# Optimization experiments

Hardware: AMD Instinct MI355X
Metric: run time of the kernel (lower is better)

## Reference

```python
import jax, jax.numpy as jnp
import numpy as np

B, IN, OUT = 512, 4096, 11008


def setup_inputs() -> dict:
    key = jax.random.key(0)
    k_x, k_stored, k_sign, k_scale, k_bias = jax.random.split(key, 5)
    x = jax.random.normal(k_x, (B, IN), dtype=jnp.float32)
    # QINS encoding: stored uint8 magnitude in [1, 255], sign in {-1, +1}
    stored = jax.random.randint(k_stored, (OUT, IN), 1, 256, dtype=jnp.int32)
    sign = 2 * jax.random.randint(k_sign, (OUT, IN), 0, 2, dtype=jnp.int32) - 1
    # log-range from from_linear's fallback calibration: weights in [e^-10, e^0]
    log_min = jnp.asarray(-10.0, dtype=jnp.float32)
    log_max = jnp.asarray(0.0, dtype=jnp.float32)
    # per-channel calibration scale, clamped to [0.5, 2.0] in from_linear
    scale = jax.random.uniform(k_scale, (OUT,), dtype=jnp.float32, minval=0.5, maxval=2.0)
    bias = jax.random.normal(k_bias, (OUT,), dtype=jnp.float32) * 0.01
    return {"x": x, "stored": stored, "sign": sign, "log_min": log_min,
            "log_max": log_max, "scale": scale, "bias": bias}


def reference(x, stored, sign, log_min, log_max, scale, bias):
    # Reconstruct fp32 weight from log-scale uint8 encoding (QINS)
    normalized = (255.0 - stored.astype(jnp.float32)) / 254.0      # [OUT, IN]
    log_w = log_min + normalized * (log_max - log_min)
    weight = sign.astype(jnp.float32) * jnp.exp(log_w)             # [OUT, IN]
    # y = (x @ W^T + b) * scale   (per-output-channel scale)
    out = jnp.einsum('bi,oi->bo', x, weight) + bias
    return out * scale
```

## Files before the change

### kernel.cpp

```cpp
#include <hip/hip_runtime.h>
#include <hip/hip_bf16.h>

#define B_DIM   512
#define IN_DIM  4096
#define OUT_DIM 11008

typedef __bf16 bf16x4  __attribute__((ext_vector_type(4)));
typedef __bf16 bf16x8  __attribute__((ext_vector_type(8)));
typedef float  floatx4 __attribute__((ext_vector_type(4)));
typedef int    intx4   __attribute__((ext_vector_type(4)));

__global__ __launch_bounds__(256) void conv_x_kernel(
    const float* __restrict__ x, __bf16* __restrict__ xb) {
  int idx = blockIdx.x * blockDim.x + threadIdx.x;
  float4 v = ((const float4*)x)[idx];
  bf16x4 o;
  o[0] = (__bf16)v.x; o[1] = (__bf16)v.y; o[2] = (__bf16)v.z; o[3] = (__bf16)v.w;
  ((bf16x4*)xb)[idx] = o;
}

__global__ __launch_bounds__(256, 2) void fused_gemm_kernel(
    const __bf16* __restrict__ A,
    const int* __restrict__ stored,
    const int* __restrict__ sign,
    const float* __restrict__ logmin, const float* __restrict__ logmax,
    const float* __restrict__ scale, const float* __restrict__ bias,
    float* __restrict__ out) {
  constexpr int K = IN_DIM, N = OUT_DIM;
  constexpr int BK = 32;

  __shared__ __align__(16) __bf16 sA[2][512 * BK];
  __shared__ __align__(16) __bf16 sB[2][32 * BK];

  const int tid  = threadIdx.x;
  const int lane = tid & 63;
  const int wave = tid >> 6;
  const int m16  = lane & 15;
  const int q    = lane >> 4;

  const int bn0 = blockIdx.x * 32;

  const float lmin  = logmin[0];
  const float slope = (logmax[0] - lmin) * (1.0f / 254.0f);

  const int ar = tid >> 2;
  const int ac = (tid & 3) * 8;
  const __bf16* gA = A + (size_t)ar * K + ac;
  const int lA = ar * BK + ac;

  const int br = tid >> 3;
  const int bc = (tid & 7) * 4;
  const int* gS = stored + (size_t)(bn0 + br) * K + bc;
  const int* gG = sign   + (size_t)(bn0 + br) * K + bc;
  const int lB = br * BK + bc;

  floatx4 acc[8][2] = {};

#define DECODE_STORE(sv, gv, dst)                                              \
  {                                                                            \
    bf16x4 wv;                                                                 \
    wv[0] = (__bf16)(__expf(fmaf((float)(255 - (sv).x), slope, lmin)) *        \
                     (float)(gv).x);                                           \
    wv[1] = (__bf16)(__expf(fmaf((float)(255 - (sv).y), slope, lmin)) *        \
                     (float)(gv).y);                                           \
    wv[2] = (__bf16)(__expf(fmaf((float)(255 - (sv).z), slope, lmin)) *        \
                     (float)(gv).z);                                           \
    wv[3] = (__bf16)(__expf(fmaf((float)(255 - (sv).w), slope, lmin)) *        \
                     (float)(gv).w);                                           \
    *(bf16x4*)(dst) = wv;                                                      \
  }

  {
    intx4 sv = __builtin_nontemporal_load((const intx4*)gS);
    intx4 gv = __builtin_nontemporal_load((const intx4*)gG);
#pragma unroll
    for (int j = 0; j < 8; ++j) {
      bf16x8 av = *(const bf16x8*)(gA + (size_t)(j * 64) * K);
      *(bf16x8*)&sA[0][lA + j * 64 * BK] = av;
    }
    DECODE_STORE(sv, gv, &sB[0][lB]);
  }
  intx4 s0 = __builtin_nontemporal_load((const intx4*)(gS + BK));
  intx4 g0 = __builtin_nontemporal_load((const intx4*)(gG + BK));
  intx4 s1 = __builtin_nontemporal_load((const intx4*)(gS + 2 * BK));
  intx4 g1 = __builtin_nontemporal_load((const intx4*)(gG + 2 * BK));

  int p = 0;
  for (int kt = 0; kt < K; kt += BK, p ^= 1) {
    __syncthreads();

    const int ktA = (kt + BK) < K ? (kt + BK) : 0;
    const int ktI = (kt + 3 * BK) < K ? (kt + 3 * BK) : 0;

    bf16x8 av[8];
#pragma unroll
    for (int j = 0; j < 8; ++j)
      av[j] = *(const bf16x8*)(gA + (size_t)(j * 64) * K + ktA);

    bf16x8 afr[8], bfr[2];
#pragma unroll
    for (int i = 0; i < 8; ++i)
      afr[i] = *(const bf16x8*)&sA[p][(wave * 128 + i * 16 + m16) * BK + q * 8];
#pragma unroll
    for (int i = 0; i < 2; ++i)
      bfr[i] = *(const bf16x8*)&sB[p][(i * 16 + m16) * BK + q * 8];

    DECODE_STORE(s0, g0, &sB[p ^ 1][lB]);
    s0 = s1; g0 = g1;
    s1 = __builtin_nontemporal_load((const intx4*)(gS + ktI));
    g1 = __builtin_nontemporal_load((const intx4*)(gG + ktI));

#pragma unroll
    for (int mi = 0; mi < 8; ++mi)
#pragma unroll
      for (int ni = 0; ni < 2; ++ni)
        acc[mi][ni] = __builtin_amdgcn_mfma_f32_16x16x32_bf16(
            afr[mi], bfr[ni], acc[mi][ni], 0, 0, 0);

#pragma unroll
    for (int j = 0; j < 8; ++j)
      *(bf16x8*)&sA[p ^ 1][lA + j * 64 * BK] = av[j];
  }

#pragma unroll
  for (int ni = 0; ni < 2; ++ni) {
    const int col = bn0 + ni * 16 + m16;
    const float sc = scale[col];
    const float bb = bias[col] * sc;
#pragma unroll
    for (int mi = 0; mi < 8; ++mi) {
#pragma unroll
      for (int r = 0; r < 4; ++r) {
        const int row = wave * 128 + mi * 16 + q * 4 + r;
        out[(size_t)row * N + col] = acc[mi][ni][r] * sc + bb;
      }
    }
  }
#undef DECODE_STORE
}

extern "C" void kernel_launch(void* const* d_in, const int* in_sizes, int n_in,
                              void* d_out, int out_size, void* d_ws, size_t ws_size,
                              hipStream_t stream) {
  const float* x      = (const float*)d_in[0];
  const int*   stored = (const int*)d_in[1];
  const int*   sign   = (const int*)d_in[2];
  const float* logmin = (const float*)d_in[3];
  const float* logmax = (const float*)d_in[4];
  const float* scale  = (const float*)d_in[5];
  const float* bias   = (const float*)d_in[6];
  float* out = (float*)d_out;

  __bf16* wsX = (__bf16*)d_ws;

  conv_x_kernel<<<(B_DIM * (IN_DIM / 4)) / 256, 256, 0, stream>>>(x, wsX);
  fused_gemm_kernel<<<OUT_DIM / 32, 256, 0, stream>>>(
      wsX, stored, sign, logmin, logmax, scale, bias, out);
}
```

Measured before the change: 510.8 us.

## Pre-swizzle activations into MFMA fragment order and read them directly from global

The conversion kernel now writes bf16 activations in MFMA fragment order, so each lane's 8-element A fragment is one contiguous 16-byte load. The GEMM kernel drops the A shared-memory staging and reads fragments straight from global/L2. It also widens the K tile for the decoded weights to 128 with padded LDS rows, cutting barriers per K. In exchange, A traffic now depends on L2/cache hits rather than LDS reuse, and the weight loads are issued only one tile ahead, so prefetch depth is shallower.

```diff
diff --git a/kernel.cpp b/kernel.cpp
--- a/kernel.cpp
+++ b/kernel.cpp
@@ -10,27 +10,32 @@
 typedef float  floatx4 __attribute__((ext_vector_type(4)));
 typedef int    intx4   __attribute__((ext_vector_type(4)));
 
-__global__ __launch_bounds__(256) void conv_x_kernel(
-    const float* __restrict__ x, __bf16* __restrict__ xb) {
-  int idx = blockIdx.x * blockDim.x + threadIdx.x;
-  float4 v = ((const float4*)x)[idx];
-  bf16x4 o;
-  o[0] = (__bf16)v.x; o[1] = (__bf16)v.y; o[2] = (__bf16)v.z; o[3] = (__bf16)v.w;
-  ((bf16x4*)xb)[idx] = o;
+__global__ __launch_bounds__(256) void conv_reorder_kernel(
+    const float* __restrict__ x, __bf16* __restrict__ Af) {
+  int t = blockIdx.x * 256 + threadIdx.x;
+  int lane = t & 63, tile = t >> 6;
+  int mt = tile & 31, kidx = tile >> 5;
+  int m16 = lane & 15, q = lane >> 4;
+  const float* src = x + (size_t)(mt * 16 + m16) * IN_DIM + kidx * 32 + q * 8;
+  float4 a = *(const float4*)src;
+  float4 b = *(const float4*)(src + 4);
+  bf16x8 o;
+  o[0] = (__bf16)a.x; o[1] = (__bf16)a.y; o[2] = (__bf16)a.z; o[3] = (__bf16)a.w;
+  o[4] = (__bf16)b.x; o[5] = (__bf16)b.y; o[6] = (__bf16)b.z; o[7] = (__bf16)b.w;
+  ((bf16x8*)Af)[t] = o;
 }
 
 __global__ __launch_bounds__(256, 2) void fused_gemm_kernel(
-    const __bf16* __restrict__ A,
+    const __bf16* __restrict__ Af,
     const int* __restrict__ stored,
     const int* __restrict__ sign,
     const float* __restrict__ logmin, const float* __restrict__ logmax,
     const float* __restrict__ scale, const float* __restrict__ bias,
     float* __restrict__ out) {
   constexpr int K = IN_DIM, N = OUT_DIM;
-  constexpr int BK = 32;
+  constexpr int SBS = 136;
 
-  __shared__ __align__(16) __bf16 sA[2][512 * BK];
-  __shared__ __align__(16) __bf16 sB[2][32 * BK];
+  __shared__ __align__(16) __bf16 sB[2][32 * SBS];
 
   const int tid  = threadIdx.x;
   const int lane = tid & 63;
@@ -43,83 +48,78 @@
   const float lmin  = logmin[0];
   const float slope = (logmax[0] - lmin) * (1.0f / 254.0f);
 
-  const int ar = tid >> 2;
-  const int ac = (tid & 3) * 8;
-  const __bf16* gA = A + (size_t)ar * K + ac;
-  const int lA = ar * BK + ac;
+  const int r  = tid >> 3;
+  const int kb = (tid & 7) * 16;
+  const int* gS = stored + (size_t)(bn0 + r) * K + kb;
+  const int* gG = sign   + (size_t)(bn0 + r) * K + kb;
 
-  const int br = tid >> 3;
-  const int bc = (tid & 7) * 4;
-  const int* gS = stored + (size_t)(bn0 + br) * K + bc;
-  const int* gG = sign   + (size_t)(bn0 + br) * K + bc;
-  const int lB = br * BK + bc;
+  const __bf16* gA = Af + (size_t)(wave * 8) * 512 + (size_t)lane * 8;
 
   floatx4 acc[8][2] = {};
 
-#define DECODE_STORE(sv, gv, dst)                                              \
-  {                                                                            \
-    bf16x4 wv;                                                                 \
-    wv[0] = (__bf16)(__expf(fmaf((float)(255 - (sv).x), slope, lmin)) *        \
-                     (float)(gv).x);                                           \
-    wv[1] = (__bf16)(__expf(fmaf((float)(255 - (sv).y), slope, lmin)) *        \
-                     (float)(gv).y);                                           \
-    wv[2] = (__bf16)(__expf(fmaf((float)(255 - (sv).z), slope, lmin)) *        \
-                     (float)(gv).z);                                           \
-    wv[3] = (__bf16)(__expf(fmaf((float)(255 - (sv).w), slope, lmin)) *        \
-                     (float)(gv).w);                                           \
-    *(bf16x4*)(dst) = wv;                                                      \
+#define DEC4(sv, gv, wv, base)                                                 \
+  wv[base + 0] = (__bf16)(__expf(fmaf((float)(255 - (sv).x), slope, lmin)) *   \
+                          (float)(gv).x);                                      \
+  wv[base + 1] = (__bf16)(__expf(fmaf((float)(255 - (sv).y), slope, lmin)) *   \
+                          (float)(gv).y);                                      \
+  wv[base + 2] = (__bf16)(__expf(fmaf((float)(255 - (sv).z), slope, lmin)) *   \
+                          (float)(gv).z);                                      \
+  wv[base + 3] = (__bf16)(__expf(fmaf((float)(255 - (sv).w), slope, lmin)) *   \
+                          (float)(gv).w)
+
+  intx4 sv[4], gv[4];
+
+#pragma unroll
+  for (int j = 0; j < 4; ++j) {
+    sv[j] = __builtin_nontemporal_load((const intx4*)(gS + j * 4));
+    gv[j] = __builtin_nontemporal_load((const intx4*)(gG + j * 4));
+  }
+  {
+    bf16x8 w0, w1;
+    DEC4(sv[0], gv[0], w0, 0); DEC4(sv[1], gv[1], w0, 4);
+    DEC4(sv[2], gv[2], w1, 0); DEC4(sv[3], gv[3], w1, 4);
+    *(bf16x8*)&sB[0][r * SBS + kb]     = w0;
+    *(bf16x8*)&sB[0][r * SBS + kb + 8] = w1;
   }
 
-  {
-    intx4 sv = __builtin_nontemporal_load((const intx4*)gS);
-    intx4 gv = __builtin_nontemporal_load((const intx4*)gG);
-#pragma unroll
-    for (int j = 0; j < 8; ++j) {
-      bf16x8 av = *(const bf16x8*)(gA + (size_t)(j * 64) * K);
-      *(bf16x8*)&sA[0][lA + j * 64 * BK] = av;
-    }
-    DECODE_STORE(sv, gv, &sB[0][lB]);
-  }
-  intx4 s0 = __builtin_nontemporal_load((const intx4*)(gS + BK));
-  intx4 g0 = __builtin_nontemporal_load((const intx4*)(gG + BK));
-  intx4 s1 = __builtin_nontemporal_load((const intx4*)(gS + 2 * BK));
-  intx4 g1 = __builtin_nontemporal_load((const intx4*)(gG + 2 * BK));
-
   int p = 0;
-  for (int kt = 0; kt < K; kt += BK, p ^= 1) {
+  for (int it = 0; it < 32; ++it, p ^= 1) {
     __syncthreads();
 
-    const int ktA = (kt + BK) < K ? (kt + BK) : 0;
-    const int ktI = (kt + 3 * BK) < K ? (kt + 3 * BK) : 0;
-
-    bf16x8 av[8];
-#pragma unroll
-    for (int j = 0; j < 8; ++j)
-      av[j] = *(const bf16x8*)(gA + (size_t)(j * 64) * K + ktA);
-
-    bf16x8 afr[8], bfr[2];
-#pragma unroll
-    for (int i = 0; i < 8; ++i)
-      afr[i] = *(const bf16x8*)&sA[p][(wave * 128 + i * 16 + m16) * BK + q * 8];
-#pragma unroll
-    for (int i = 0; i < 2; ++i)
-      bfr[i] = *(const bf16x8*)&sB[p][(i * 16 + m16) * BK + q * 8];
-
-    DECODE_STORE(s0, g0, &sB[p ^ 1][lB]);
-    s0 = s1; g0 = g1;
-    s1 = __builtin_nontemporal_load((const intx4*)(gS + ktI));
-    g1 = __builtin_nontemporal_load((const intx4*)(gG + ktI));
+    const bool more = (it + 1) < 32;
+    const int  ktn  = more ? (it + 1) * 128 : 0;
 
 #pragma unroll
-    for (int mi = 0; mi < 8; ++mi)
+    for (int j = 0; j < 4; ++j) {
+      sv[j] = __builtin_nontemporal_load((const intx4*)(gS + ktn + j * 4));
+      gv[j] = __builtin_nontemporal_load((const intx4*)(gG + ktn + j * 4));
+    }
+
+#pragma unroll
+    for (int kk = 0; kk < 4; ++kk) {
+      const int kidx = it * 4 + kk;
+      bf16x8 afr[8], bfr[2];
+#pragma unroll
+      for (int mi = 0; mi < 8; ++mi)
+        afr[mi] = *(const bf16x8*)(gA + ((size_t)kidx * 32 + mi) * 512);
 #pragma unroll
       for (int ni = 0; ni < 2; ++ni)
-        acc[mi][ni] = __builtin_amdgcn_mfma_f32_16x16x32_bf16(
-            afr[mi], bfr[ni], acc[mi][ni], 0, 0, 0);
+        bfr[ni] = *(const bf16x8*)&sB[p][(ni * 16 + m16) * SBS + kk * 32 + q * 8];
+#pragma unroll
+      for (int mi = 0; mi < 8; ++mi)
+#pragma unroll
+        for (int ni = 0; ni < 2; ++ni)
+          acc[mi][ni] = __builtin_amdgcn_mfma_f32_16x16x32_bf16(
+              afr[mi], bfr[ni], acc[mi][ni], 0, 0, 0);
+    }
 
-#pragma unroll
-    for (int j = 0; j < 8; ++j)
-      *(bf16x8*)&sA[p ^ 1][lA + j * 64 * BK] = av[j];
+    if (more) {
+      bf16x8 w0, w1;
+      DEC4(sv[0], gv[0], w0, 0); DEC4(sv[1], gv[1], w0, 4);
+      DEC4(sv[2], gv[2], w1, 0); DEC4(sv[3], gv[3], w1, 4);
+      *(bf16x8*)&sB[p ^ 1][r * SBS + kb]     = w0;
+      *(bf16x8*)&sB[p ^ 1][r * SBS + kb + 8] = w1;
+    }
   }
 
 #pragma unroll
@@ -130,13 +130,13 @@
 #pragma unroll
     for (int mi = 0; mi < 8; ++mi) {
 #pragma unroll
-      for (int r = 0; r < 4; ++r) {
-        const int row = wave * 128 + mi * 16 + q * 4 + r;
-        out[(size_t)row * N + col] = acc[mi][ni][r] * sc + bb;
+      for (int rr = 0; rr < 4; ++rr) {
+        const int row = wave * 128 + mi * 16 + q * 4 + rr;
+        out[(size_t)row * N + col] = acc[mi][ni][rr] * sc + bb;
       }
     }
   }
-#undef DECODE_STORE
+#undef DEC4
 }
 
 extern "C" void kernel_launch(void* const* d_in, const int* in_sizes, int n_in,
@@ -151,9 +151,9 @@
   const float* bias   = (const float*)d_in[6];
   float* out = (float*)d_out;
 
-  __bf16* wsX = (__bf16*)d_ws;
+  __bf16* wsAf = (__bf16*)d_ws;
 
-  conv_x_kernel<<<(B_DIM * (IN_DIM / 4)) / 256, 256, 0, stream>>>(x, wsX);
+  conv_reorder_kernel<<<(B_DIM * IN_DIM / 8) / 256, 256, 0, stream>>>(x, wsAf);
   fused_gemm_kernel<<<OUT_DIM / 32, 256, 0, stream>>>(
-      wsX, stored, sign, logmin, logmax, scale, bias, out);
+      wsAf, stored, sign, logmin, logmax, scale, bias, out);
 }
```

New measurement: 482.1 us. 1.06x faster.
